# Kernel optimization log

Measured on AMD Instinct MI355X. Metric: run time of the kernel, lower is better.

Reference implementation:

```python
import jax, jax.numpy as jnp
import numpy as np

BSZ, SEQ, HID = 4, 4096, 2048
NUM_EXPERTS, TOPK = 64, 8


def setup_inputs() -> dict:
    key = jax.random.key(0)
    kx, kw = jax.random.split(key)
    x = jax.random.normal(kx, (BSZ, SEQ, HID), dtype=jnp.float32)
    # nn.Linear default init scale ~ 1/sqrt(fan_in); exact init irrelevant for correctness baseline
    W = jax.random.normal(kw, (NUM_EXPERTS, HID), dtype=jnp.float32) * (HID ** -0.5)
    b = jnp.zeros((NUM_EXPERTS,), dtype=jnp.float32)
    return {"x": x, "W": W, "b": b}


def reference(x, W, b):
    # gate: (bsz, seq, num_experts)
    gate = jnp.einsum("bsh,eh->bse", x, W) + b
    # top-k along expert dim
    logits, ids = jax.lax.top_k(gate, TOPK)  # (bsz, seq, topk)
    # scatter top-k logits into a -inf mask, then softmax over all experts
    bsz, seq, ne = gate.shape
    bi = jnp.arange(bsz)[:, None, None]
    si = jnp.arange(seq)[None, :, None]
    mask = jnp.full(gate.shape, -jnp.inf, dtype=gate.dtype)
    mask = mask.at[bi, si, ids].set(logits)
    probs = jax.nn.softmax(mask, axis=-1)  # zeros outside top-k
    return (probs, ids)
```

## Files before the change

kernel.cpp:

```cpp
#include <hip/hip_runtime.h>
#include <math.h>

#define BSZ 4
#define SEQ 4096
#define HID 2048
#define NE 64
#define TOPK 8
#define NTOK (BSZ*SEQ)
#define NSPLIT 4
#define KSPL (HID/NSPLIT)
#define KC 64
#define BT 64

#define XS 80
#define WS2 80

typedef double f64x4 __attribute__((ext_vector_type(4)));

__global__ __launch_bounds__(256, 4)
void moe_gate_gemm(const float* __restrict__ x, const float* __restrict__ W,
                   float* __restrict__ part) {
    __shared__ float xlds[KC * XS];
    __shared__ float wlds2[KC * WS2];

    const int tid   = threadIdx.x;
    const int tile  = blockIdx.x;
    const int split = blockIdx.y;
    const int T0 = tile * BT;
    const int k0 = split * KSPL;

    const int wv   = tid >> 6;
    const int lane = tid & 63;
    const int kof  = lane >> 4;
    const int col  = lane & 15;

    const int srow = tid & 63;

    const double a1 = (kof == 0) ? (double)col : 0.0;
    const double b1 = (kof == 0) ? 1.0 : 0.0;
    const double a2 = (kof == 0) ? 1.0 : 0.0;
    const double b2 = (kof == 0) ? (double)col : 0.0;
    const f64x4 zero = (f64x4){0.0, 0.0, 0.0, 0.0};
    const f64x4 cal1 = __builtin_amdgcn_mfma_f64_16x16x4f64(a1, b1, zero, 0, 0, 0);
    const f64x4 cal2 = __builtin_amdgcn_mfma_f64_16x16x4f64(a2, b2, zero, 0, 0, 0);
    int drow[4], dcol[4];
    #pragma unroll
    for (int a = 0; a < 4; a++) {
        drow[a] = (int)cal1[a];
        dcol[a] = (int)cal2[a];
    }

    f64x4 acc[4];
    #pragma unroll
    for (int nt = 0; nt < 4; nt++) acc[nt] = zero;

    const int base_a = kof * XS  + wv * 16 + col;
    const int base_b = kof * WS2 + col * 4;

    float4 px[4], pw[4];
    #pragma unroll
    for (int r = 0; r < 4; r++) {
        const int k4 = wv * 4 + r;
        px[r] = *reinterpret_cast<const float4*>(&x[(size_t)(T0 + srow) * HID + k0 + k4 * 4]);
        pw[r] = *reinterpret_cast<const float4*>(&W[(size_t)srow  * HID + k0 + k4 * 4]);
    }

    const int wcol = (srow & 15) * 4 + (srow >> 4);

    for (int c = 0; c < KSPL / KC; c++) {
        __syncthreads();
        #pragma unroll
        for (int r = 0; r < 4; r++) {
            const int k4 = wv * 4 + r;
            xlds[(k4 * 4 + 0) * XS + srow] = px[r].x;
            xlds[(k4 * 4 + 1) * XS + srow] = px[r].y;
            xlds[(k4 * 4 + 2) * XS + srow] = px[r].z;
            xlds[(k4 * 4 + 3) * XS + srow] = px[r].w;
            wlds2[(k4 * 4 + 0) * WS2 + wcol] = pw[r].x;
            wlds2[(k4 * 4 + 1) * WS2 + wcol] = pw[r].y;
            wlds2[(k4 * 4 + 2) * WS2 + wcol] = pw[r].z;
            wlds2[(k4 * 4 + 3) * WS2 + wcol] = pw[r].w;
        }
        if (c + 1 < KSPL / KC) {
            const int kc = k0 + (c + 1) * KC;
            #pragma unroll
            for (int r = 0; r < 4; r++) {
                const int k4 = wv * 4 + r;
                px[r] = *reinterpret_cast<const float4*>(&x[(size_t)(T0 + srow) * HID + kc + k4 * 4]);
                pw[r] = *reinterpret_cast<const float4*>(&W[(size_t)srow  * HID + kc + k4 * 4]);
            }
        }
        __syncthreads();

        #pragma unroll
        for (int kb = 0; kb < KC / 4; kb++) {
            const double ad = (double)xlds[kb * (4 * XS) + base_a];
            const float4 bf = *reinterpret_cast<const float4*>(&wlds2[kb * (4 * WS2) + base_b]);
            acc[0] = __builtin_amdgcn_mfma_f64_16x16x4f64(ad, (double)bf.x, acc[0], 0, 0, 0);
            acc[1] = __builtin_amdgcn_mfma_f64_16x16x4f64(ad, (double)bf.y, acc[1], 0, 0, 0);
            acc[2] = __builtin_amdgcn_mfma_f64_16x16x4f64(ad, (double)bf.z, acc[2], 0, 0, 0);
            acc[3] = __builtin_amdgcn_mfma_f64_16x16x4f64(ad, (double)bf.w, acc[3], 0, 0, 0);
        }
    }

    #pragma unroll
    for (int nt = 0; nt < 4; nt++) {
        #pragma unroll
        for (int a = 0; a < 4; a++) {
            const int tok = T0 + wv * 16 + drow[a];
            const int e   = nt * 16 + dcol[a];
            part[((size_t)split * NTOK + tok) * NE + e] = (float)acc[nt][a];
        }
    }
}

__global__ __launch_bounds__(256)
void moe_topk_softmax(const float* __restrict__ part, const float* __restrict__ b,
                      float* __restrict__ probs, float* __restrict__ ids) {
    const int lane  = threadIdx.x & 63;
    const int w     = threadIdx.x >> 6;
    const int token = blockIdx.x * 4 + w;

    float g = b[lane];
    #pragma unroll
    for (int s = 0; s < NSPLIT; s++)
        g += part[((size_t)s * NTOK + token) * NE + lane];

    const float gorig = g;
    float cur = g;
    float m = 0.f, denom = 0.f;
    int   myid = 0;
    bool  sel = false;

    #pragma unroll
    for (int it = 0; it < TOPK; it++) {
        float v = cur;
        int idx = lane;
        #pragma unroll
        for (int d = 1; d < 64; d <<= 1) {
            const float ov = __shfl_xor(v, d, 64);
            const int   oi = __shfl_xor(idx, d, 64);
            if (ov > v || (ov == v && oi < idx)) { v = ov; idx = oi; }
        }
        if (it == 0) m = v;
        denom += expf(v - m);
        if (lane == idx) { sel = true; cur = -INFINITY; }
        if (lane == it)  myid = idx;
    }

    probs[(size_t)token * NE + lane] = sel ? expf(gorig - m) / denom : 0.f;
    if (lane < TOPK) ids[(size_t)token * TOPK + lane] = (float)myid;
}

extern "C" void kernel_launch(void* const* d_in, const int* in_sizes, int n_in,
                              void* d_out, int out_size, void* d_ws, size_t ws_size,
                              hipStream_t stream) {
    const float* x = (const float*)d_in[0];
    const float* W = (const float*)d_in[1];
    const float* b = (const float*)d_in[2];

    float* probs = (float*)d_out;
    float* ids   = (float*)d_out + (size_t)NTOK * NE;
    float* part  = (float*)d_ws;

    dim3 g1(NTOK / BT, NSPLIT);
    moe_gate_gemm<<<g1, 256, 0, stream>>>(x, W, part);
    moe_topk_softmax<<<NTOK / 4, 256, 0, stream>>>(part, b, probs, ids);
}
```

Baseline: 248.4 us.

## Double-buffer LDS stages in gate GEMM with one barrier per chunk

Halves the K chunk to 32 and ping-pongs between two LDS buffers. The next chunk is written to the idle buffer while MFMAs consume the current one, which drops one of the two __syncthreads per chunk. It also raises wave priority around the MFMA loop with s_setprio. In exchange there are twice as many iterations and half as many loads in flight per thread, which could reduce memory-level parallelism in this bandwidth-bound kernel.

```diff
diff --git a/kernel.cpp b/kernel.cpp
--- a/kernel.cpp
+++ b/kernel.cpp
@@ -9,19 +9,22 @@
 #define NTOK (BSZ*SEQ)
 #define NSPLIT 4
 #define KSPL (HID/NSPLIT)
-#define KC 64
+#define KC 32
+#define NCH (KSPL/KC)
 #define BT 64
 
 #define XS 80
 #define WS2 80
+#define XBUF (KC*XS)
+#define WBUF (KC*WS2)
 
 typedef double f64x4 __attribute__((ext_vector_type(4)));
 
 __global__ __launch_bounds__(256, 4)
 void moe_gate_gemm(const float* __restrict__ x, const float* __restrict__ W,
                    float* __restrict__ part) {
-    __shared__ float xlds[KC * XS];
-    __shared__ float wlds2[KC * WS2];
+    __shared__ float xlds[2 * XBUF];
+    __shared__ float wlds2[2 * WBUF];
 
     const int tid   = threadIdx.x;
     const int tile  = blockIdx.x;
@@ -35,6 +38,7 @@
     const int col  = lane & 15;
 
     const int srow = tid & 63;
+    const int wcol = (srow & 15) * 4 + (srow >> 4);
 
     const double a1 = (kof == 0) ? (double)col : 0.0;
     const double b1 = (kof == 0) ? 1.0 : 0.0;
@@ -57,49 +61,68 @@
     const int base_a = kof * XS  + wv * 16 + col;
     const int base_b = kof * WS2 + col * 4;
 
-    float4 px[4], pw[4];
-    #pragma unroll
-    for (int r = 0; r < 4; r++) {
-        const int k4 = wv * 4 + r;
-        px[r] = *reinterpret_cast<const float4*>(&x[(size_t)(T0 + srow) * HID + k0 + k4 * 4]);
-        pw[r] = *reinterpret_cast<const float4*>(&W[(size_t)srow  * HID + k0 + k4 * 4]);
+    float4 px[2], pw[2];
+
+#define STAGE_LOAD(KOFF)                                                              \
+    {                                                                                 \
+        _Pragma("unroll")                                                             \
+        for (int r = 0; r < 2; r++) {                                                 \
+            const int k4 = wv * 2 + r;                                                \
+            px[r] = *reinterpret_cast<const float4*>(                                 \
+                &x[(size_t)(T0 + srow) * HID + (KOFF) + k4 * 4]);                     \
+            pw[r] = *reinterpret_cast<const float4*>(                                 \
+                &W[(size_t)srow * HID + (KOFF) + k4 * 4]);                            \
+        }                                                                             \
     }
 
-    const int wcol = (srow & 15) * 4 + (srow >> 4);
+#define STAGE_WRITE(XB, WB)                                                           \
+    {                                                                                 \
+        _Pragma("unroll")                                                             \
+        for (int r = 0; r < 2; r++) {                                                 \
+            const int k4 = wv * 2 + r;                                                \
+            xlds[(XB) + (k4 * 4 + 0) * XS + srow] = px[r].x;                          \
+            xlds[(XB) + (k4 * 4 + 1) * XS + srow] = px[r].y;                          \
+            xlds[(XB) + (k4 * 4 + 2) * XS + srow] = px[r].z;                          \
+            xlds[(XB) + (k4 * 4 + 3) * XS + srow] = px[r].w;                          \
+            wlds2[(WB) + (k4 * 4 + 0) * WS2 + wcol] = pw[r].x;                        \
+            wlds2[(WB) + (k4 * 4 + 1) * WS2 + wcol] = pw[r].y;                        \
+            wlds2[(WB) + (k4 * 4 + 2) * WS2 + wcol] = pw[r].z;                        \
+            wlds2[(WB) + (k4 * 4 + 3) * WS2 + wcol] = pw[r].w;                        \
+        }                                                                             \
+    }
 
-    for (int c = 0; c < KSPL / KC; c++) {
+#define COMPUTE(XB, WB)                                                               \
+    {                                                                                 \
+        __builtin_amdgcn_s_setprio(1);                                                \
+        _Pragma("unroll")                                                             \
+        for (int kb = 0; kb < KC / 4; kb++) {                                         \
+            const double ad = (double)xlds[(XB) + kb * (4 * XS) + base_a];            \
+            const float4 bf = *reinterpret_cast<const float4*>(                       \
+                &wlds2[(WB) + kb * (4 * WS2) + base_b]);                              \
+            acc[0] = __builtin_amdgcn_mfma_f64_16x16x4f64(ad, (double)bf.x, acc[0], 0, 0, 0); \
+            acc[1] = __builtin_amdgcn_mfma_f64_16x16x4f64(ad, (double)bf.y, acc[1], 0, 0, 0); \
+            acc[2] = __builtin_amdgcn_mfma_f64_16x16x4f64(ad, (double)bf.z, acc[2], 0, 0, 0); \
+            acc[3] = __builtin_amdgcn_mfma_f64_16x16x4f64(ad, (double)bf.w, acc[3], 0, 0, 0); \
+        }                                                                             \
+        __builtin_amdgcn_s_setprio(0);                                                \
+    }
+
+    STAGE_LOAD(k0);
+    STAGE_WRITE(0, 0);
+    STAGE_LOAD(k0 + KC);
+    __syncthreads();
+
+    for (int t = 0; t < NCH / 2; ++t) {
+        const int c0 = 2 * t;
+        COMPUTE(0, 0);
+        STAGE_WRITE(XBUF, WBUF);
+        if (c0 + 2 < NCH) STAGE_LOAD(k0 + (c0 + 2) * KC);
         __syncthreads();
-        #pragma unroll
-        for (int r = 0; r < 4; r++) {
-            const int k4 = wv * 4 + r;
-            xlds[(k4 * 4 + 0) * XS + srow] = px[r].x;
-            xlds[(k4 * 4 + 1) * XS + srow] = px[r].y;
-            xlds[(k4 * 4 + 2) * XS + srow] = px[r].z;
-            xlds[(k4 * 4 + 3) * XS + srow] = px[r].w;
-            wlds2[(k4 * 4 + 0) * WS2 + wcol] = pw[r].x;
-            wlds2[(k4 * 4 + 1) * WS2 + wcol] = pw[r].y;
-            wlds2[(k4 * 4 + 2) * WS2 + wcol] = pw[r].z;
-            wlds2[(k4 * 4 + 3) * WS2 + wcol] = pw[r].w;
-        }
-        if (c + 1 < KSPL / KC) {
-            const int kc = k0 + (c + 1) * KC;
-            #pragma unroll
-            for (int r = 0; r < 4; r++) {
-                const int k4 = wv * 4 + r;
-                px[r] = *reinterpret_cast<const float4*>(&x[(size_t)(T0 + srow) * HID + kc + k4 * 4]);
-                pw[r] = *reinterpret_cast<const float4*>(&W[(size_t)srow  * HID + kc + k4 * 4]);
-            }
-        }
-        __syncthreads();
-
-        #pragma unroll
-        for (int kb = 0; kb < KC / 4; kb++) {
-            const double ad = (double)xlds[kb * (4 * XS) + base_a];
-            const float4 bf = *reinterpret_cast<const float4*>(&wlds2[kb * (4 * WS2) + base_b]);
-            acc[0] = __builtin_amdgcn_mfma_f64_16x16x4f64(ad, (double)bf.x, acc[0], 0, 0, 0);
-            acc[1] = __builtin_amdgcn_mfma_f64_16x16x4f64(ad, (double)bf.y, acc[1], 0, 0, 0);
-            acc[2] = __builtin_amdgcn_mfma_f64_16x16x4f64(ad, (double)bf.z, acc[2], 0, 0, 0);
-            acc[3] = __builtin_amdgcn_mfma_f64_16x16x4f64(ad, (double)bf.w, acc[3], 0, 0, 0);
+        COMPUTE(XBUF, WBUF);
+        if (c0 + 2 < NCH) {
+            STAGE_WRITE(0, 0);
+            if (c0 + 3 < NCH) STAGE_LOAD(k0 + (c0 + 3) * KC);
+            __syncthreads();
         }
     }
 
@@ -112,6 +135,9 @@
             part[((size_t)split * NTOK + tok) * NE + e] = (float)acc[nt][a];
         }
     }
+#undef STAGE_LOAD
+#undef STAGE_WRITE
+#undef COMPUTE
 }
 
 __global__ __launch_bounds__(256)
```

After: 245.1 us. No clear change (-1.3%).
